# Optimization experiments

Measured on AMD Instinct MI355X. Metric: run time of the kernel, lower is better.

## Reference

```python
import jax, jax.numpy as jnp
import numpy as np

L, H, C, V, T_MAX = 12, 12, 768, 50257, 1024
D = C // H
LN_EPS = 1e-5


def layer_norm(x, w, b):
    m = jnp.mean(x, axis=-1, keepdims=True)
    v = jnp.mean(jnp.square(x - m), axis=-1, keepdims=True)
    return (x - m) * jax.lax.rsqrt(v + LN_EPS) * w + b


def setup_inputs() -> dict:
    key = jax.random.key(0)
    ks = jax.random.split(key, 16)
    B, T = 2, 1024
    s = 0.02
    inp = {
        "idx": jax.random.randint(ks[0], (B, T), 0, V),
        "wte": jax.random.normal(ks[1], (V, C), jnp.float32) * s,
        "wpe": jax.random.normal(ks[2], (T_MAX, C), jnp.float32) * s,
        # stacked per-layer params, leading axis = layer
        "ln1_w": jnp.ones((L, C), jnp.float32),
        "ln1_b": jnp.zeros((L, C), jnp.float32),
        "Wq": jax.random.normal(ks[3], (L, C, C), jnp.float32) * s,
        "bq": jnp.zeros((L, C), jnp.float32),
        "Wk": jax.random.normal(ks[4], (L, C, C), jnp.float32) * s,
        "bk": jnp.zeros((L, C), jnp.float32),
        "Wv": jax.random.normal(ks[5], (L, C, C), jnp.float32) * s,
        "bv": jnp.zeros((L, C), jnp.float32),
        "Wo": jax.random.normal(ks[6], (L, C, C), jnp.float32) * (s / np.sqrt(2 * L)),
        "bo": jnp.zeros((L, C), jnp.float32),
        "ln2_w": jnp.ones((L, C), jnp.float32),
        "ln2_b": jnp.zeros((L, C), jnp.float32),
        "Wfc": jax.random.normal(ks[7], (L, C, 4 * C), jnp.float32) * s,
        "bfc": jnp.zeros((L, 4 * C), jnp.float32),
        "Wpr": jax.random.normal(ks[8], (L, 4 * C, C), jnp.float32) * (s / np.sqrt(2 * L)),
        "bpr": jnp.zeros((L, C), jnp.float32),
        "ln_f_w": jnp.ones((C,), jnp.float32),
        "ln_f_b": jnp.zeros((C,), jnp.float32),
        "Wlm": jax.random.normal(ks[9], (C, V), jnp.float32) * s,
    }
    return inp


def _forward(idx, wte, wpe, ln1_w, ln1_b, Wq, bq, Wk, bk, Wv, bv, Wo, bo,
             ln2_w, ln2_b, Wfc, bfc, Wpr, bpr, ln_f_w, ln_f_b, Wlm):
    B, T = idx.shape
    x = wte[idx] + wpe[jnp.arange(T)][None, :, :]  # (B,T,C)
    causal = jnp.tril(jnp.ones((T, T), bool))  # (T,T) causal mask
    scale = 1.0 / np.sqrt(D)
    neg_inf = jnp.finfo(x.dtype).min

    def block(x, p):
        (l1w, l1b, wq, bq_, wk, bk_, wv, bv_, wo, bo_,
         l2w, l2b, wfc, bfc_, wpr, bpr_) = p
        h = layer_norm(x, l1w, l1b)
        q = (h @ wq + bq_).reshape(B, T, H, D)
        k = (h @ wk + bk_).reshape(B, T, H, D)
        v = (h @ wv + bv_).reshape(B, T, H, D)
        scores = jnp.einsum("bqhd,bkhd->bhqk", q, k) * scale
        scores = jnp.where(causal[None, None], scores, neg_inf)
        attn = jax.nn.softmax(scores, axis=-1)
        y = jnp.einsum("bhqk,bkhd->bqhd", attn, v).reshape(B, T, C)
        x = x + y @ wo + bo_
        h2 = layer_norm(x, l2w, l2b)
        x = x + jax.nn.gelu(h2 @ wfc + bfc_, approximate=False) @ wpr + bpr_
        return x, None

    params = (ln1_w, ln1_b, Wq, bq, Wk, bk, Wv, bv, Wo, bo,
              ln2_w, ln2_b, Wfc, bfc, Wpr, bpr)
    x, _ = jax.lax.scan(block, x, params)
    x = layer_norm(x, ln_f_w, ln_f_b)
    logits = x @ Wlm  # (B,T,V)
    return logits


def reference(idx, wte, wpe, ln1_w, ln1_b, Wq, bq, Wk, bk, Wv, bv, Wo, bo,
              ln2_w, ln2_b, Wfc, bfc, Wpr, bpr, ln_f_w, ln_f_b, Wlm):
    return _forward(idx, wte, wpe, ln1_w, ln1_b, Wq, bq, Wk, bk, Wv, bv, Wo, bo,
                    ln2_w, ln2_b, Wfc, bfc, Wpr, bpr, ln_f_w, ln_f_b, Wlm)
```

## Files before the change

### kernel.cpp

```cpp
#include <hip/hip_runtime.h>
#include <math.h>
#include <cstddef>


#define Cdim 768
#define Hn   12
#define Ln   12
#define Tn   1024
#define Bn   2
#define Mrows (Bn * Tn)

typedef unsigned short ushort_t;
typedef __bf16 bf16x8 __attribute__((ext_vector_type(8)));
typedef float  f32x4  __attribute__((ext_vector_type(4)));

__device__ __forceinline__ ushort_t f2bf(float v) {
    union { float f; unsigned int u; } x; x.f = v;
    unsigned int r = x.u + 0x7fffu + ((x.u >> 16) & 1u);
    return (ushort_t)(r >> 16);
}
__device__ __forceinline__ float gelu_f(float v) {
    return 0.5f * v * (1.0f + erff(v * 0.70710678118654752f));
}
__device__ __forceinline__ void gload16(const void* g, void* l) {
    __builtin_amdgcn_global_load_lds(
        (const __attribute__((address_space(1))) unsigned int*)g,
        (__attribute__((address_space(3))) unsigned int*)l, 16, 0, 0);
}

__global__ void embed_k(const int* __restrict__ idx, const float* __restrict__ wte,
                        const float* __restrict__ wpe, float* __restrict__ x) {
    int i = blockIdx.x * 256 + threadIdx.x;
    int c  = i % Cdim;
    int bt = i / Cdim;
    int t  = bt % Tn;
    int tok = idx[bt];
    x[i] = wte[(size_t)tok * Cdim + c] + wpe[(size_t)t * Cdim + c];
}

__global__ __launch_bounds__(256) void ln_k(const float* __restrict__ x,
                                            const float* __restrict__ w,
                                            const float* __restrict__ b,
                                            ushort_t* __restrict__ out) {
    int row = blockIdx.x;
    const float* xr = x + (size_t)row * Cdim;
    int t = threadIdx.x;
    float v0 = xr[t], v1 = xr[t + 256], v2 = xr[t + 512];
    float s = v0 + v1 + v2;
    #pragma unroll
    for (int o = 32; o > 0; o >>= 1) s += __shfl_xor(s, o);
    __shared__ float red[8];
    int wid = t >> 6;
    if ((t & 63) == 0) red[wid] = s;
    __syncthreads();
    float mean = (red[0] + red[1] + red[2] + red[3]) * (1.0f / 768.0f);
    float d0 = v0 - mean, d1 = v1 - mean, d2 = v2 - mean;
    float sq = d0 * d0 + d1 * d1 + d2 * d2;
    #pragma unroll
    for (int o = 32; o > 0; o >>= 1) sq += __shfl_xor(sq, o);
    if ((t & 63) == 0) red[4 + wid] = sq;
    __syncthreads();
    float var = (red[4] + red[5] + red[6] + red[7]) * (1.0f / 768.0f);
    float rstd = rsqrtf(var + 1e-5f);
    ushort_t* orow = out + (size_t)row * Cdim;
    orow[t]       = f2bf(d0 * rstd * w[t]       + b[t]);
    orow[t + 256] = f2bf(d1 * rstd * w[t + 256] + b[t + 256]);
    orow[t + 512] = f2bf(d2 * rstd * w[t + 512] + b[t + 512]);
}

__device__ __forceinline__ void tconv_tile(const float* __restrict__ W,
                                           ushort_t* __restrict__ WT,
                                           int K, int N, int n0, int k0, bool guard) {
    __shared__ float t[32][33];
    int x = threadIdx.x & 31, y = threadIdx.x >> 5;
    #pragma unroll
    for (int j = 0; j < 4; ++j) {
        int kk = k0 + y + j * 8, nn = n0 + x;
        t[y + j * 8][x] = (!guard || nn < N) ? W[(size_t)kk * N + nn] : 0.0f;
    }
    __syncthreads();
    #pragma unroll
    for (int j = 0; j < 4; ++j) {
        int nn = n0 + y + j * 8, kk = k0 + x;
        WT[(size_t)nn * K + kk] = f2bf(t[x][y + j * 8]);
    }
}

__global__ __launch_bounds__(256) void wconv_k(const float* __restrict__ W,
                                               ushort_t* __restrict__ WT,
                                               int K, int N) {
    tconv_tile(W, WT, K, N, blockIdx.x * 32, blockIdx.y * 32, true);
}

__global__ __launch_bounds__(256) void conv_layer_k(
    const float* __restrict__ Wq, const float* __restrict__ Wk,
    const float* __restrict__ Wv, const float* __restrict__ Wo,
    const float* __restrict__ Wfc, const float* __restrict__ Wpr,
    const float* __restrict__ bq, const float* __restrict__ bk,
    const float* __restrict__ bv,
    ushort_t* __restrict__ wqkvt, ushort_t* __restrict__ wot,
    ushort_t* __restrict__ wfct,  ushort_t* __restrict__ wprt,
    float* __restrict__ bqkv) {
    int bid = blockIdx.x;
    if (bid < 2304) {
        int z = bid / 576, t = bid % 576;
        const float* W = (z == 0) ? Wq : (z == 1) ? Wk : (z == 2) ? Wv : Wo;
        ushort_t* dst = (z < 3) ? (wqkvt + (size_t)z * 768 * 768) : wot;
        tconv_tile(W, dst, 768, 768, (t % 24) * 32, (t / 24) * 32, false);
    } else if (bid < 4608) {
        int t = bid - 2304;
        tconv_tile(Wfc, wfct, 768, 3072, (t % 96) * 32, (t / 96) * 32, false);
    } else if (bid < 6912) {
        int t = bid - 4608;
        tconv_tile(Wpr, wprt, 3072, 768, (t % 24) * 32, (t / 24) * 32, false);
    } else {
        int i = (bid - 6912) * 256 + threadIdx.x;
        bqkv[i] = (i < 768) ? bq[i] : (i < 1536 ? bk[i - 768] : bv[i - 1536]);
    }
}

template <bool BIAS, bool GELU_, bool RES, bool OUTBF16, int MODE>
__global__ __launch_bounds__(256) void gemm_bf16_k(
    const ushort_t* __restrict__ A, const ushort_t* __restrict__ Bt,
    const float* __restrict__ bias, const float* __restrict__ res,
    void* __restrict__ Cout, int M, int N, int K, int cpx) {
    __shared__ ushort_t Alds[2][128 * 32];
    __shared__ ushort_t Blds[2][128 * 32];
    const int tid = threadIdx.x;
    const int lane = tid & 63;
    const int w = tid >> 6;
    const int wr = w >> 1, wc = w & 1;
    int m0, n0;
    if (MODE == 2) {
        int lid = (blockIdx.x & 7) * cpx + (blockIdx.x >> 3);
        m0 = (lid & 15) * 128;
        n0 = (lid >> 4) * 128;
    } else {
        m0 = blockIdx.y * 128;
        n0 = blockIdx.x * 128;
    }

    f32x4 acc[4][4] = {};
    const int srow = w * 32 + (lane >> 2);
    const int skoff = (lane & 3) * 8;
    const ushort_t* Ab = A  + (size_t)(m0 + srow) * K + skoff;
    const ushort_t* Bb = Bt + (size_t)(n0 + srow) * K + skoff;
    char* Al0 = (char*)&Alds[0][0] + (w * 2048 + lane * 16);
    char* Al1 = (char*)&Alds[1][0] + (w * 2048 + lane * 16);
    char* Bl0 = (char*)&Blds[0][0] + (w * 2048 + lane * 16);
    char* Bl1 = (char*)&Blds[1][0] + (w * 2048 + lane * 16);

    const int nk = K >> 6;
    for (int kb = 0; kb < nk; ++kb) {
        const int k0 = kb << 6;
        __syncthreads();
        gload16(Ab + k0,                       Al0);
        gload16(Ab + k0 + (size_t)16 * K,      Al0 + 1024);
        gload16(Ab + k0 + 32,                  Al1);
        gload16(Ab + k0 + 32 + (size_t)16 * K, Al1 + 1024);
        gload16(Bb + k0,                       Bl0);
        gload16(Bb + k0 + (size_t)16 * K,      Bl0 + 1024);
        gload16(Bb + k0 + 32,                  Bl1);
        gload16(Bb + k0 + 32 + (size_t)16 * K, Bl1 + 1024);
        __syncthreads();
        #pragma unroll
        for (int h = 0; h < 2; ++h) {
            bf16x8 af[4], bfr[4];
            #pragma unroll
            for (int i = 0; i < 4; ++i) {
                af[i]  = *(const bf16x8*)((const char*)&Alds[h][0] +
                           ((wr * 64 + i * 16 + (lane & 15)) * 64 + (lane >> 4) * 16));
                bfr[i] = *(const bf16x8*)((const char*)&Blds[h][0] +
                           ((wc * 64 + i * 16 + (lane & 15)) * 64 + (lane >> 4) * 16));
            }
            #pragma unroll
            for (int mi = 0; mi < 4; ++mi)
                #pragma unroll
                for (int ni = 0; ni < 4; ++ni)
                    acc[mi][ni] = __builtin_amdgcn_mfma_f32_16x16x32_bf16(
                        af[mi], bfr[ni], acc[mi][ni], 0, 0, 0);
        }
    }
    const int r0 = (lane >> 4) * 4;
    const int c0 = lane & 15;
    #pragma unroll
    for (int mi = 0; mi < 4; ++mi) {
        #pragma unroll
        for (int ni = 0; ni < 4; ++ni) {
            int col = n0 + wc * 64 + ni * 16 + c0;
            if (col < N) {
                #pragma unroll
                for (int q = 0; q < 4; ++q) {
                    int row = m0 + wr * 64 + mi * 16 + r0 + q;
                    float v = acc[mi][ni][q];
                    if (BIAS) v += bias[col];
                    if (GELU_) v = gelu_f(v);
                    if (RES) v += res[(size_t)row * N + col];
                    if (OUTBF16) ((ushort_t*)Cout)[(size_t)row * N + col] = f2bf(v);
                    else         ((float*)Cout)[(size_t)row * N + col] = v;
                }
            }
        }
    }
}

template <bool BIAS, bool RES>
__global__ __launch_bounds__(256) void gemm64_k(
    const ushort_t* __restrict__ A, const ushort_t* __restrict__ Bt,
    const float* __restrict__ bias, const float* __restrict__ res,
    float* __restrict__ Cout, int M, int N, int K) {
    __shared__ ushort_t Alds[4][64 * 32];
    __shared__ ushort_t Blds[4][64 * 32];
    const int tid = threadIdx.x;
    const int lane = tid & 63;
    const int w = tid >> 6;
    const int wr = w >> 1, wc = w & 1;
    const int m0 = blockIdx.y * 64;
    const int n0 = blockIdx.x * 64;

    f32x4 acc[2][2] = {};
    const int srow = w * 16 + (lane >> 2);
    const int skoff = (lane & 3) * 8;
    const ushort_t* Ab = A  + (size_t)(m0 + srow) * K + skoff;
    const ushort_t* Bb = Bt + (size_t)(n0 + srow) * K + skoff;

    const int nk = K >> 7;
    for (int kb = 0; kb < nk; ++kb) {
        const int k0 = kb << 7;
        __syncthreads();
        #pragma unroll
        for (int s = 0; s < 4; ++s) {
            gload16(Ab + k0 + s * 32, (char*)&Alds[s][0] + (w * 1024 + lane * 16));
            gload16(Bb + k0 + s * 32, (char*)&Blds[s][0] + (w * 1024 + lane * 16));
        }
        __syncthreads();
        #pragma unroll
        for (int s = 0; s < 4; ++s) {
            bf16x8 af[2], bfr[2];
            #pragma unroll
            for (int i = 0; i < 2; ++i) {
                af[i]  = *(const bf16x8*)((const char*)&Alds[s][0] +
                           ((wr * 32 + i * 16 + (lane & 15)) * 64 + (lane >> 4) * 16));
                bfr[i] = *(const bf16x8*)((const char*)&Blds[s][0] +
                           ((wc * 32 + i * 16 + (lane & 15)) * 64 + (lane >> 4) * 16));
            }
            #pragma unroll
            for (int mi = 0; mi < 2; ++mi)
                #pragma unroll
                for (int ni = 0; ni < 2; ++ni)
                    acc[mi][ni] = __builtin_amdgcn_mfma_f32_16x16x32_bf16(
                        af[mi], bfr[ni], acc[mi][ni], 0, 0, 0);
        }
    }
    const int r0 = (lane >> 4) * 4;
    const int c0 = lane & 15;
    #pragma unroll
    for (int mi = 0; mi < 2; ++mi)
        #pragma unroll
        for (int ni = 0; ni < 2; ++ni) {
            int col = n0 + wc * 32 + ni * 16 + c0;
            #pragma unroll
            for (int q = 0; q < 4; ++q) {
                int row = m0 + wr * 32 + mi * 16 + r0 + q;
                float v = acc[mi][ni][q];
                if (BIAS) v += bias[col];
                if (RES) v += res[(size_t)row * N + col];
                Cout[(size_t)row * N + col] = v;
            }
        }
}

__global__ __launch_bounds__(256) void kvprep_k(const ushort_t* __restrict__ qkvb,
                                                ushort_t* __restrict__ kpb,
                                                ushort_t* __restrict__ vtb) {
    __shared__ ushort_t Ls[256][72];
    const int tc = blockIdx.x, h = blockIdx.y, b = blockIdx.z;
    const int tid = threadIdx.x;
    const int tok = tc * 256 + tid;
    const ushort_t* base = qkvb + (size_t)(b * Tn + tok) * 2304 + h * 64;
    ushort_t* kdst = kpb + ((size_t)(b * Hn + h) * Tn + tok) * 64;
    #pragma unroll
    for (int i = 0; i < 8; ++i)
        *(uint4*)&kdst[i * 8] = *(const uint4*)(base + 768 + i * 8);
    #pragma unroll
    for (int i = 0; i < 8; ++i)
        *(uint4*)&Ls[tid][i * 8] = *(const uint4*)(base + 1536 + i * 8);
    __syncthreads();
    const int d = tid & 63, tg = tid >> 6;
    ushort_t tmp[64];
    #pragma unroll
    for (int i = 0; i < 64; ++i) tmp[i] = Ls[tg * 64 + i][d];
    ushort_t* dst = vtb + ((size_t)(b * Hn + h) * 64 + d) * Tn + tc * 256 + tg * 64;
    #pragma unroll
    for (int i = 0; i < 8; ++i)
        *(uint4*)&dst[i * 8] = *(const uint4*)&tmp[i * 8];
}

__global__ __launch_bounds__(256) void attn_mfma_k(
    const ushort_t* __restrict__ qkvb,
    const ushort_t* __restrict__ kpb,
    const ushort_t* __restrict__ vtb,
    ushort_t* __restrict__ yb) {
    __shared__ ushort_t Ks[64][72];
    __shared__ ushort_t Vt[64][72];
    __shared__ ushort_t Pl[4][16][72];
    const int chunk = (Tn / 64 - 1) - blockIdx.x;
    const int h = blockIdx.y, b = blockIdx.z;
    const int tid = threadIdx.x, lane = tid & 63, w = tid >> 6;
    const int c = lane & 15, g = lane >> 4;
    const int qrow0 = chunk * 64 + w * 16;

    const ushort_t* qp = qkvb + (size_t)(b * Tn + qrow0 + c) * 2304 + h * 64 + g * 8;
    bf16x8 qa0 = *(const bf16x8*)qp;
    bf16x8 qa1 = *(const bf16x8*)(qp + 32);

    f32x4 accO[4] = {};
    float mrun[4], lrun[4];
    #pragma unroll
    for (int q = 0; q < 4; ++q) { mrun[q] = -1e30f; lrun[q] = 0.0f; }

    const int skey = tid >> 2, sd0 = (tid & 3) * 16;
    const ushort_t* ksrc = kpb + ((size_t)(b * Hn + h) * Tn + skey) * 64 + sd0;
    const int vd = tid >> 2, vseg = tid & 3;
    const ushort_t* vsrc = vtb + ((size_t)(b * Hn + h) * 64 + vd) * Tn + vseg * 16;
    ushort_t* KsW = &Ks[skey][sd0];
    ushort_t* VtW = &Vt[vd][vseg * 16];

    const int ntiles = chunk + 1;
    for (int kt = 0; kt < ntiles; ++kt) {
        __syncthreads();
        {
            const ushort_t* kp = ksrc + (size_t)kt * 64 * 64;
            *(uint4*)KsW       = *(const uint4*)kp;
            *(uint4*)(KsW + 8) = *(const uint4*)(kp + 8);
            const ushort_t* vp = vsrc + kt * 64;
            *(uint4*)VtW       = *(const uint4*)vp;
            *(uint4*)(VtW + 8) = *(const uint4*)(vp + 8);
        }
        __syncthreads();

        f32x4 sf[4];
        #pragma unroll
        for (int nk = 0; nk < 4; ++nk) {
            bf16x8 kf0 = *(const bf16x8*)&Ks[nk * 16 + c][g * 8];
            bf16x8 kf1 = *(const bf16x8*)&Ks[nk * 16 + c][g * 8 + 32];
            f32x4 z = {};
            z = __builtin_amdgcn_mfma_f32_16x16x32_bf16(qa0, kf0, z, 0, 0, 0);
            z = __builtin_amdgcn_mfma_f32_16x16x32_bf16(qa1, kf1, z, 0, 0, 0);
            sf[nk] = z;
        }
        float pmax[4] = {-1e30f, -1e30f, -1e30f, -1e30f};
        #pragma unroll
        for (int nk = 0; nk < 4; ++nk) {
            int key = kt * 64 + nk * 16 + c;
            #pragma unroll
            for (int q = 0; q < 4; ++q) {
                float sv = sf[nk][q];
                int row = qrow0 + g * 4 + q;
                sv = (key > row) ? -1e30f : sv;
                sf[nk][q] = sv;
                pmax[q] = fmaxf(pmax[q], sv);
            }
        }
        #pragma unroll
        for (int q = 0; q < 4; ++q)
            #pragma unroll
            for (int off = 1; off < 16; off <<= 1)
                pmax[q] = fmaxf(pmax[q], __shfl_xor(pmax[q], off));
        float corr[4], psum[4];
        #pragma unroll
        for (int q = 0; q < 4; ++q) {
            float mn = fmaxf(mrun[q], pmax[q]);
            corr[q] = __expf((mrun[q] - mn) * 0.125f);
            mrun[q] = mn;
            psum[q] = 0.0f;
        }
        #pragma unroll
        for (int nk = 0; nk < 4; ++nk)
            #pragma unroll
            for (int q = 0; q < 4; ++q) {
                float p = __expf((sf[nk][q] - mrun[q]) * 0.125f);
                psum[q] += p;
                Pl[w][g * 4 + q][nk * 16 + c] = f2bf(p);
            }
        #pragma unroll
        for (int q = 0; q < 4; ++q) {
            #pragma unroll
            for (int off = 1; off < 16; off <<= 1)
                psum[q] += __shfl_xor(psum[q], off);
            lrun[q] = lrun[q] * corr[q] + psum[q];
        }
        #pragma unroll
        for (int ni = 0; ni < 4; ++ni)
            #pragma unroll
            for (int q = 0; q < 4; ++q)
                accO[ni][q] *= corr[q];

        asm volatile("" ::: "memory");
        bf16x8 pa0 = *(const bf16x8*)&Pl[w][c][g * 8];
        bf16x8 pa1 = *(const bf16x8*)&Pl[w][c][g * 8 + 32];
        #pragma unroll
        for (int ni = 0; ni < 4; ++ni) {
            bf16x8 bv0 = *(const bf16x8*)&Vt[ni * 16 + c][g * 8];
            bf16x8 bv1 = *(const bf16x8*)&Vt[ni * 16 + c][g * 8 + 32];
            accO[ni] = __builtin_amdgcn_mfma_f32_16x16x32_bf16(pa0, bv0, accO[ni], 0, 0, 0);
            accO[ni] = __builtin_amdgcn_mfma_f32_16x16x32_bf16(pa1, bv1, accO[ni], 0, 0, 0);
        }
    }

    #pragma unroll
    for (int q = 0; q < 4; ++q) {
        float inv = 1.0f / lrun[q];
        ushort_t* yr = yb + (size_t)(b * Tn + qrow0 + g * 4 + q) * Cdim + h * 64;
        #pragma unroll
        for (int ni = 0; ni < 4; ++ni)
            yr[ni * 16 + c] = f2bf(accO[ni][q] * inv);
    }
}

extern "C" void kernel_launch(void* const* d_in, const int* in_sizes, int n_in,
                              void* d_out, int out_size, void* d_ws, size_t ws_size,
                              hipStream_t stream) {
    const int*   idx  = (const int*)d_in[0];
    const float* wte  = (const float*)d_in[1];
    const float* wpe  = (const float*)d_in[2];
    const float* ln1w = (const float*)d_in[3];
    const float* ln1b = (const float*)d_in[4];
    const float* Wq   = (const float*)d_in[5];
    const float* bq   = (const float*)d_in[6];
    const float* Wk   = (const float*)d_in[7];
    const float* bk   = (const float*)d_in[8];
    const float* Wv   = (const float*)d_in[9];
    const float* bv   = (const float*)d_in[10];
    const float* Wo   = (const float*)d_in[11];
    const float* bo   = (const float*)d_in[12];
    const float* ln2w = (const float*)d_in[13];
    const float* ln2b = (const float*)d_in[14];
    const float* Wfc  = (const float*)d_in[15];
    const float* bfc  = (const float*)d_in[16];
    const float* Wpr  = (const float*)d_in[17];
    const float* bpr  = (const float*)d_in[18];
    const float* lnfw = (const float*)d_in[19];
    const float* lnfb = (const float*)d_in[20];
    const float* Wlm  = (const float*)d_in[21];
    float* out = (float*)d_out;

    const int M = Mrows;
    const int V = out_size / M;
    const int Vpad = ((V + 127) / 128) * 128;

    float*    x     = (float*)d_ws;
    float*    bqkv  = x + (size_t)M * Cdim;
    ushort_t* qkvb  = (ushort_t*)(bqkv + 2304);
    ushort_t* kpb   = qkvb + (size_t)M * 2304;
    ushort_t* vtb   = kpb + (size_t)Bn * Hn * Tn * 64;
    ushort_t* hb    = vtb + (size_t)Bn * Hn * 64 * Tn;
    ushort_t* yb    = hb + (size_t)M * Cdim;
    ushort_t* mid   = yb + (size_t)M * Cdim;
    ushort_t* wqkvt = mid + (size_t)M * 3072;
    ushort_t* wot   = wqkvt + (size_t)2304 * Cdim;
    ushort_t* wfct  = wot + (size_t)Cdim * Cdim;
    ushort_t* wprt  = wfct + (size_t)3072 * Cdim;
    ushort_t* wlmt  = wprt + (size_t)Cdim * 3072;

    embed_k<<<(M * Cdim) / 256, 256, 0, stream>>>(idx, wte, wpe, x);

    for (int l = 0; l < Ln; ++l) {
        const size_t wo2 = (size_t)l * Cdim * Cdim;
        const size_t wo4 = (size_t)l * Cdim * 4 * Cdim;
        conv_layer_k<<<6921, 256, 0, stream>>>(
            Wq + wo2, Wk + wo2, Wv + wo2, Wo + wo2, Wfc + wo4, Wpr + wo4,
            bq + l * Cdim, bk + l * Cdim, bv + l * Cdim,
            wqkvt, wot, wfct, wprt, bqkv);

        ln_k<<<M, 256, 0, stream>>>(x, ln1w + l * Cdim, ln1b + l * Cdim, hb);
        gemm_bf16_k<true, false, false, true, 0><<<dim3(18, 16), 256, 0, stream>>>(
            hb, wqkvt, bqkv, nullptr, qkvb, M, 2304, Cdim, 0);
        kvprep_k<<<dim3(4, Hn, Bn), 256, 0, stream>>>(qkvb, kpb, vtb);
        attn_mfma_k<<<dim3(16, Hn, Bn), 256, 0, stream>>>(qkvb, kpb, vtb, yb);
        gemm64_k<true, true><<<dim3(12, 32), 256, 0, stream>>>(
            yb, wot, bo + l * Cdim, x, x, M, Cdim, Cdim);
        ln_k<<<M, 256, 0, stream>>>(x, ln2w + l * Cdim, ln2b + l * Cdim, hb);
        gemm_bf16_k<true, true, false, true, 0><<<dim3(24, 16), 256, 0, stream>>>(
            hb, wfct, bfc + (size_t)l * 4 * Cdim, nullptr, mid, M, 3072, Cdim, 0);
        gemm64_k<true, true><<<dim3(12, 32), 256, 0, stream>>>(
            mid, wprt, bpr + l * Cdim, x, x, M, Cdim, 3072);
    }

    ln_k<<<M, 256, 0, stream>>>(x, lnfw, lnfb, hb);
    wconv_k<<<dim3(Vpad / 32, 24), 256, 0, stream>>>(Wlm, wlmt, Cdim, V);
    const int nblk = (Vpad / 128) * 16;
    gemm_bf16_k<false, false, false, false, 2><<<nblk, 256, 0, stream>>>(
        hb, wlmt, nullptr, nullptr, out, M, V, Cdim, nblk / 8);
}
```

Before: 2.170 ms.

## Add dedicated 256x256-tile LM-head GEMM with swizzled LDS and prefetch pipeline

Replaces the LM-head projection's 128x128-tile GEMM with a new 512-thread kernel using 256x256 tiles, 64-wide K steps, double-buffered LDS with an XOR swizzle to avoid bank conflicts, explicit vmcnt waits to overlap the next tile's loads with MFMA work, and setprio around the compute. It targets the largest GEMM (2048x50257x768), aiming for more reuse per loaded tile and better overlap of loads with compute. The generic GEMM template loses its blockIdx-remap mode. Vocab padding grows to a multiple of 256, which adds some wasted work at the edge, and the large accumulator tile raises register pressure.

```diff
diff --git a/kernel.cpp b/kernel.cpp
--- a/kernel.cpp
+++ b/kernel.cpp
@@ -119,26 +119,19 @@
     }
 }
 
-template <bool BIAS, bool GELU_, bool RES, bool OUTBF16, int MODE>
+template <bool BIAS, bool GELU_, bool RES, bool OUTBF16>
 __global__ __launch_bounds__(256) void gemm_bf16_k(
     const ushort_t* __restrict__ A, const ushort_t* __restrict__ Bt,
     const float* __restrict__ bias, const float* __restrict__ res,
-    void* __restrict__ Cout, int M, int N, int K, int cpx) {
+    void* __restrict__ Cout, int M, int N, int K) {
     __shared__ ushort_t Alds[2][128 * 32];
     __shared__ ushort_t Blds[2][128 * 32];
     const int tid = threadIdx.x;
     const int lane = tid & 63;
     const int w = tid >> 6;
     const int wr = w >> 1, wc = w & 1;
-    int m0, n0;
-    if (MODE == 2) {
-        int lid = (blockIdx.x & 7) * cpx + (blockIdx.x >> 3);
-        m0 = (lid & 15) * 128;
-        n0 = (lid >> 4) * 128;
-    } else {
-        m0 = blockIdx.y * 128;
-        n0 = blockIdx.x * 128;
-    }
+    const int m0 = blockIdx.y * 128;
+    const int n0 = blockIdx.x * 128;
 
     f32x4 acc[4][4] = {};
     const int srow = w * 32 + (lane >> 2);
@@ -202,6 +195,106 @@
             }
         }
     }
+}
+
+__global__ __launch_bounds__(512, 2) void gemm_lm_k(
+    const ushort_t* __restrict__ A,
+    const ushort_t* __restrict__ Bt,
+    float* __restrict__ Cout,
+    int M, int N, int K, int cpx) {
+    __shared__ ushort_t Asl[2][256 * 64];
+    __shared__ ushort_t Bsl[2][256 * 64];
+    const int tid = threadIdx.x;
+    const int lane = tid & 63;
+    const int w = tid >> 6;
+    const int wr = w >> 2, wc = w & 3;
+    const int lid = ((int)blockIdx.x & 7) * cpx + ((int)blockIdx.x >> 3);
+    const int m0 = (lid & 7) * 256;
+    const int n0 = (lid >> 3) * 256;
+
+    f32x4 acc[8][4] = {};
+
+    const int srow = tid >> 3;
+    const int scol = ((tid & 7) * 8) ^ (((tid >> 5) & 1) << 4);
+    const ushort_t* Asrc = A  + (size_t)(m0 + srow) * K + scol;
+    const ushort_t* Bsrc = Bt + (size_t)(n0 + srow) * K + scol;
+    const int ldsoff = tid * 16;
+
+    const int nt = K >> 6;
+    #pragma unroll
+    for (int j = 0; j < 4; ++j) {
+        gload16(Asrc + (size_t)(j * 64) * K, (char*)&Asl[0][0] + ldsoff + j * 8192);
+        gload16(Bsrc + (size_t)(j * 64) * K, (char*)&Bsl[0][0] + ldsoff + j * 8192);
+    }
+    for (int t = 0; t < nt; ++t) {
+        const int buf = t & 1;
+        if (t + 1 < nt) {
+            const int k0 = (t + 1) << 6;
+            #pragma unroll
+            for (int j = 0; j < 4; ++j) {
+                gload16(Asrc + k0 + (size_t)(j * 64) * K,
+                        (char*)&Asl[buf ^ 1][0] + ldsoff + j * 8192);
+                gload16(Bsrc + k0 + (size_t)(j * 64) * K,
+                        (char*)&Bsl[buf ^ 1][0] + ldsoff + j * 8192);
+            }
+            asm volatile("s_waitcnt vmcnt(8)" ::: "memory");
+        } else {
+            asm volatile("s_waitcnt vmcnt(0)" ::: "memory");
+        }
+        __builtin_amdgcn_sched_barrier(0);
+        __builtin_amdgcn_s_barrier();
+        asm volatile("" ::: "memory");
+
+        const char* Ab = (const char*)&Asl[buf][0];
+        const char* Bb = (const char*)&Bsl[buf][0];
+        bf16x8 bfr[4][2];
+        #pragma unroll
+        for (int n = 0; n < 4; ++n)
+            #pragma unroll
+            for (int ks = 0; ks < 2; ++ks) {
+                int row = wc * 64 + n * 16 + (lane & 15);
+                int o = row * 128 + ks * 64 + ((lane >> 4) * 16);
+                o ^= ((row >> 2) & 1) << 5;
+                bfr[n][ks] = *(const bf16x8*)(Bb + o);
+            }
+        __builtin_amdgcn_s_setprio(1);
+        #pragma unroll
+        for (int m = 0; m < 8; ++m) {
+            bf16x8 af[2];
+            #pragma unroll
+            for (int ks = 0; ks < 2; ++ks) {
+                int row = wr * 128 + m * 16 + (lane & 15);
+                int o = row * 128 + ks * 64 + ((lane >> 4) * 16);
+                o ^= ((row >> 2) & 1) << 5;
+                af[ks] = *(const bf16x8*)(Ab + o);
+            }
+            #pragma unroll
+            for (int n = 0; n < 4; ++n)
+                #pragma unroll
+                for (int ks = 0; ks < 2; ++ks)
+                    acc[m][n] = __builtin_amdgcn_mfma_f32_16x16x32_bf16(
+                        af[ks], bfr[n][ks], acc[m][n], 0, 0, 0);
+        }
+        __builtin_amdgcn_s_setprio(0);
+        asm volatile("" ::: "memory");
+        __builtin_amdgcn_sched_barrier(0);
+        __builtin_amdgcn_s_barrier();
+    }
+
+    const int r0 = (lane >> 4) * 4, c0 = lane & 15;
+    #pragma unroll
+    for (int m = 0; m < 8; ++m)
+        #pragma unroll
+        for (int n = 0; n < 4; ++n) {
+            int col = n0 + wc * 64 + n * 16 + c0;
+            if (col < N) {
+                #pragma unroll
+                for (int q = 0; q < 4; ++q) {
+                    int row = m0 + wr * 128 + m * 16 + r0 + q;
+                    Cout[(size_t)row * N + col] = acc[m][n][q];
+                }
+            }
+        }
 }
 
 template <bool BIAS, bool RES>
@@ -447,7 +540,7 @@
 
     const int M = Mrows;
     const int V = out_size / M;
-    const int Vpad = ((V + 127) / 128) * 128;
+    const int Vpad = ((V + 255) / 256) * 256;
 
     float*    x     = (float*)d_ws;
     float*    bqkv  = x + (size_t)M * Cdim;
@@ -474,22 +567,21 @@
             wqkvt, wot, wfct, wprt, bqkv);
 
         ln_k<<<M, 256, 0, stream>>>(x, ln1w + l * Cdim, ln1b + l * Cdim, hb);
-        gemm_bf16_k<true, false, false, true, 0><<<dim3(18, 16), 256, 0, stream>>>(
-            hb, wqkvt, bqkv, nullptr, qkvb, M, 2304, Cdim, 0);
+        gemm_bf16_k<true, false, false, true><<<dim3(18, 16), 256, 0, stream>>>(
+            hb, wqkvt, bqkv, nullptr, qkvb, M, 2304, Cdim);
         kvprep_k<<<dim3(4, Hn, Bn), 256, 0, stream>>>(qkvb, kpb, vtb);
         attn_mfma_k<<<dim3(16, Hn, Bn), 256, 0, stream>>>(qkvb, kpb, vtb, yb);
         gemm64_k<true, true><<<dim3(12, 32), 256, 0, stream>>>(
             yb, wot, bo + l * Cdim, x, x, M, Cdim, Cdim);
         ln_k<<<M, 256, 0, stream>>>(x, ln2w + l * Cdim, ln2b + l * Cdim, hb);
-        gemm_bf16_k<true, true, false, true, 0><<<dim3(24, 16), 256, 0, stream>>>(
-            hb, wfct, bfc + (size_t)l * 4 * Cdim, nullptr, mid, M, 3072, Cdim, 0);
+        gemm_bf16_k<true, true, false, true><<<dim3(24, 16), 256, 0, stream>>>(
+            hb, wfct, bfc + (size_t)l * 4 * Cdim, nullptr, mid, M, 3072, Cdim);
         gemm64_k<true, true><<<dim3(12, 32), 256, 0, stream>>>(
             mid, wprt, bpr + l * Cdim, x, x, M, Cdim, 3072);
     }
 
     ln_k<<<M, 256, 0, stream>>>(x, lnfw, lnfb, hb);
     wconv_k<<<dim3(Vpad / 32, 24), 256, 0, stream>>>(Wlm, wlmt, Cdim, V);
-    const int nblk = (Vpad / 128) * 16;
-    gemm_bf16_k<false, false, false, false, 2><<<nblk, 256, 0, stream>>>(
-        hb, wlmt, nullptr, nullptr, out, M, V, Cdim, nblk / 8);
-}
+    const int nblk = (Vpad / 256) * 8;
+    gemm_lm_k<<<nblk, 512, 0, stream>>>(hb, wlmt, out, M, V, Cdim, nblk / 8);
+}
```

Result: no change. 2.195 ms (+1.1%).

## Replace bf16 GEMM with double-buffered pipelined kernel and larger LM-head tiles

Applied to the files above, without the earlier changes.

Replaces the 128x128 bf16 GEMM with a templated kernel that prefetches the next K tile into a second LDS buffer while MFMAs run on the current one. It uses an XOR-swizzled LDS layout to avoid bank conflicts, raw s_barrier with vmcnt waits, and s_setprio around the MFMA loop. The LM-head GEMM moves to 256x256 tiles with 512 threads and XCD-aware block remapping, and Vpad is padded to 256. The larger tiles use more LDS and registers, which lowers occupancy and adds padding waste on the vocab dimension.

```diff
diff --git a/kernel.cpp b/kernel.cpp
--- a/kernel.cpp
+++ b/kernel.cpp
@@ -119,89 +119,120 @@
     }
 }
 
-template <bool BIAS, bool GELU_, bool RES, bool OUTBF16, int MODE>
-__global__ __launch_bounds__(256) void gemm_bf16_k(
-    const ushort_t* __restrict__ A, const ushort_t* __restrict__ Bt,
-    const float* __restrict__ bias, const float* __restrict__ res,
-    void* __restrict__ Cout, int M, int N, int K, int cpx) {
-    __shared__ ushort_t Alds[2][128 * 32];
-    __shared__ ushort_t Blds[2][128 * 32];
+template <int BM, int BN, int TH, int WGN, bool BIAS, bool GELU_, bool OUTBF16, bool XCD>
+__global__ __launch_bounds__(TH, 2) void gemm_pipe_k(
+    const ushort_t* __restrict__ A,
+    const ushort_t* __restrict__ Bt,
+    const float* __restrict__ bias,
+    void* __restrict__ Cout,
+    int M, int N, int K, int cpx, int mtiles) {
+    constexpr int SA = BM * 128;
+    constexpr int SB = BN * 128;
+    constexpr int WM = BM / 2;
+    constexpr int WN = BN / WGN;
+    constexpr int FM = WM / 16;
+    constexpr int FN = WN / 16;
+    constexpr int RJ = TH / 8;
+    __shared__ char lds[2 * (SA + SB)];
+    char* Abase = lds;
+    char* Bbase = lds + 2 * SA;
+
     const int tid = threadIdx.x;
     const int lane = tid & 63;
     const int w = tid >> 6;
-    const int wr = w >> 1, wc = w & 1;
+    const int wr = w / WGN, wc = w % WGN;
     int m0, n0;
-    if (MODE == 2) {
-        int lid = (blockIdx.x & 7) * cpx + (blockIdx.x >> 3);
-        m0 = (lid & 15) * 128;
-        n0 = (lid >> 4) * 128;
+    if (XCD) {
+        int lid = ((int)blockIdx.x & 7) * cpx + ((int)blockIdx.x >> 3);
+        m0 = (lid % mtiles) * BM;
+        n0 = (lid / mtiles) * BN;
     } else {
-        m0 = blockIdx.y * 128;
-        n0 = blockIdx.x * 128;
-    }
-
-    f32x4 acc[4][4] = {};
-    const int srow = w * 32 + (lane >> 2);
-    const int skoff = (lane & 3) * 8;
-    const ushort_t* Ab = A  + (size_t)(m0 + srow) * K + skoff;
-    const ushort_t* Bb = Bt + (size_t)(n0 + srow) * K + skoff;
-    char* Al0 = (char*)&Alds[0][0] + (w * 2048 + lane * 16);
-    char* Al1 = (char*)&Alds[1][0] + (w * 2048 + lane * 16);
-    char* Bl0 = (char*)&Blds[0][0] + (w * 2048 + lane * 16);
-    char* Bl1 = (char*)&Blds[1][0] + (w * 2048 + lane * 16);
-
-    const int nk = K >> 6;
-    for (int kb = 0; kb < nk; ++kb) {
-        const int k0 = kb << 6;
-        __syncthreads();
-        gload16(Ab + k0,                       Al0);
-        gload16(Ab + k0 + (size_t)16 * K,      Al0 + 1024);
-        gload16(Ab + k0 + 32,                  Al1);
-        gload16(Ab + k0 + 32 + (size_t)16 * K, Al1 + 1024);
-        gload16(Bb + k0,                       Bl0);
-        gload16(Bb + k0 + (size_t)16 * K,      Bl0 + 1024);
-        gload16(Bb + k0 + 32,                  Bl1);
-        gload16(Bb + k0 + 32 + (size_t)16 * K, Bl1 + 1024);
-        __syncthreads();
-        #pragma unroll
-        for (int h = 0; h < 2; ++h) {
-            bf16x8 af[4], bfr[4];
-            #pragma unroll
-            for (int i = 0; i < 4; ++i) {
-                af[i]  = *(const bf16x8*)((const char*)&Alds[h][0] +
-                           ((wr * 64 + i * 16 + (lane & 15)) * 64 + (lane >> 4) * 16));
-                bfr[i] = *(const bf16x8*)((const char*)&Blds[h][0] +
-                           ((wc * 64 + i * 16 + (lane & 15)) * 64 + (lane >> 4) * 16));
+        m0 = blockIdx.y * BM;
+        n0 = blockIdx.x * BN;
+    }
+
+    f32x4 acc[FM][FN] = {};
+
+    const int srowl = tid >> 3;
+    const int sslot = (tid & 7) ^ (srowl & 7);
+    const ushort_t* Asrc = A  + (size_t)(m0 + srowl) * K + sslot * 8;
+    const ushort_t* Bsrc = Bt + (size_t)(n0 + srowl) * K + sslot * 8;
+
+    auto stageall = [&](int d, int kt) {
+        const ushort_t* As = Asrc + kt * 64;
+        const ushort_t* Bs = Bsrc + kt * 64;
+        #pragma unroll
+        for (int j = 0; j < 4; ++j) {
+            gload16(As + (size_t)(j * RJ) * K, Abase + d * SA + tid * 16 + j * (TH * 16));
+            gload16(Bs + (size_t)(j * RJ) * K, Bbase + d * SB + tid * 16 + j * (TH * 16));
+        }
+    };
+    auto readA = [&](int d, int m, int ks) -> bf16x8 {
+        int rl = wr * WM + m * 16 + (lane & 15);
+        int s  = ks * 4 + (lane >> 4);
+        return *(const bf16x8*)(Abase + d * SA + rl * 128 + ((s ^ (rl & 7)) << 4));
+    };
+    auto readB = [&](int d, int n, int ks) -> bf16x8 {
+        int rl = wc * WN + n * 16 + (lane & 15);
+        int s  = ks * 4 + (lane >> 4);
+        return *(const bf16x8*)(Bbase + d * SB + rl * 128 + ((s ^ (rl & 7)) << 4));
+    };
+
+    const int nt = K >> 6;
+    stageall(0, 0);
+    for (int kt = 0; kt < nt; ++kt) {
+        const int d = kt & 1;
+        if (kt + 1 < nt) {
+            stageall(d ^ 1, kt + 1);
+            asm volatile("s_waitcnt vmcnt(8)" ::: "memory");
+        } else {
+            asm volatile("s_waitcnt vmcnt(0)" ::: "memory");
+        }
+        __builtin_amdgcn_s_barrier();
+        asm volatile("" ::: "memory");
+
+        bf16x8 bfr[FN][2];
+        #pragma unroll
+        for (int n = 0; n < FN; ++n) {
+            bfr[n][0] = readB(d, n, 0);
+            bfr[n][1] = readB(d, n, 1);
+        }
+        __builtin_amdgcn_s_setprio(1);
+        #pragma unroll
+        for (int m = 0; m < FM; ++m) {
+            bf16x8 a0 = readA(d, m, 0);
+            bf16x8 a1 = readA(d, m, 1);
+            #pragma unroll
+            for (int n = 0; n < FN; ++n) {
+                acc[m][n] = __builtin_amdgcn_mfma_f32_16x16x32_bf16(
+                    a0, bfr[n][0], acc[m][n], 0, 0, 0);
+                acc[m][n] = __builtin_amdgcn_mfma_f32_16x16x32_bf16(
+                    a1, bfr[n][1], acc[m][n], 0, 0, 0);
             }
-            #pragma unroll
-            for (int mi = 0; mi < 4; ++mi)
-                #pragma unroll
-                for (int ni = 0; ni < 4; ++ni)
-                    acc[mi][ni] = __builtin_amdgcn_mfma_f32_16x16x32_bf16(
-                        af[mi], bfr[ni], acc[mi][ni], 0, 0, 0);
-        }
-    }
-    const int r0 = (lane >> 4) * 4;
-    const int c0 = lane & 15;
-    #pragma unroll
-    for (int mi = 0; mi < 4; ++mi) {
-        #pragma unroll
-        for (int ni = 0; ni < 4; ++ni) {
-            int col = n0 + wc * 64 + ni * 16 + c0;
+        }
+        __builtin_amdgcn_s_setprio(0);
+        asm volatile("" ::: "memory");
+        __builtin_amdgcn_s_barrier();
+    }
+
+    const int r0 = (lane >> 4) * 4, c0 = lane & 15;
+    #pragma unroll
+    for (int m = 0; m < FM; ++m)
+        #pragma unroll
+        for (int n = 0; n < FN; ++n) {
+            int col = n0 + wc * WN + n * 16 + c0;
             if (col < N) {
                 #pragma unroll
                 for (int q = 0; q < 4; ++q) {
-                    int row = m0 + wr * 64 + mi * 16 + r0 + q;
-                    float v = acc[mi][ni][q];
+                    int row = m0 + wr * WM + m * 16 + r0 + q;
+                    float v = acc[m][n][q];
                     if (BIAS) v += bias[col];
                     if (GELU_) v = gelu_f(v);
-                    if (RES) v += res[(size_t)row * N + col];
                     if (OUTBF16) ((ushort_t*)Cout)[(size_t)row * N + col] = f2bf(v);
                     else         ((float*)Cout)[(size_t)row * N + col] = v;
                 }
             }
         }
-    }
 }
 
 template <bool BIAS, bool RES>
@@ -447,7 +478,7 @@
 
     const int M = Mrows;
     const int V = out_size / M;
-    const int Vpad = ((V + 127) / 128) * 128;
+    const int Vpad = ((V + 255) / 256) * 256;
 
     float*    x     = (float*)d_ws;
     float*    bqkv  = x + (size_t)M * Cdim;
@@ -474,22 +505,25 @@
             wqkvt, wot, wfct, wprt, bqkv);
 
         ln_k<<<M, 256, 0, stream>>>(x, ln1w + l * Cdim, ln1b + l * Cdim, hb);
-        gemm_bf16_k<true, false, false, true, 0><<<dim3(18, 16), 256, 0, stream>>>(
-            hb, wqkvt, bqkv, nullptr, qkvb, M, 2304, Cdim, 0);
+        gemm_pipe_k<128, 128, 256, 2, true, false, true, false>
+            <<<dim3(18, 16), 256, 0, stream>>>(
+            hb, wqkvt, bqkv, qkvb, M, 2304, Cdim, 0, 0);
         kvprep_k<<<dim3(4, Hn, Bn), 256, 0, stream>>>(qkvb, kpb, vtb);
         attn_mfma_k<<<dim3(16, Hn, Bn), 256, 0, stream>>>(qkvb, kpb, vtb, yb);
         gemm64_k<true, true><<<dim3(12, 32), 256, 0, stream>>>(
             yb, wot, bo + l * Cdim, x, x, M, Cdim, Cdim);
         ln_k<<<M, 256, 0, stream>>>(x, ln2w + l * Cdim, ln2b + l * Cdim, hb);
-        gemm_bf16_k<true, true, false, true, 0><<<dim3(24, 16), 256, 0, stream>>>(
-            hb, wfct, bfc + (size_t)l * 4 * Cdim, nullptr, mid, M, 3072, Cdim, 0);
+        gemm_pipe_k<128, 128, 256, 2, true, true, true, false>
+            <<<dim3(24, 16), 256, 0, stream>>>(
+            hb, wfct, bfc + (size_t)l * 4 * Cdim, mid, M, 3072, Cdim, 0, 0);
         gemm64_k<true, true><<<dim3(12, 32), 256, 0, stream>>>(
             mid, wprt, bpr + l * Cdim, x, x, M, Cdim, 3072);
     }
 
     ln_k<<<M, 256, 0, stream>>>(x, lnfw, lnfb, hb);
     wconv_k<<<dim3(Vpad / 32, 24), 256, 0, stream>>>(Wlm, wlmt, Cdim, V);
-    const int nblk = (Vpad / 128) * 16;
-    gemm_bf16_k<false, false, false, false, 2><<<nblk, 256, 0, stream>>>(
-        hb, wlmt, nullptr, nullptr, out, M, V, Cdim, nblk / 8);
-}
+    const int nblk = (Vpad / 256) * 8;
+    gemm_pipe_k<256, 256, 512, 4, false, false, false, true>
+        <<<nblk, 512, 0, stream>>>(
+        hb, wlmt, nullptr, out, M, V, Cdim, nblk / 8, 8);
+}
```

New measurement: 2.045 ms. 1.06x faster.
